# Kernel optimization log

Measured on AMD Instinct MI355X. Metric: run time of the kernel, lower is better.

## Reference

```python
import jax, jax.numpy as jnp
import numpy as np

B, N, D = 4, 1024, 1024      # batch, seq_len, query_dim
H, DH = 16, 64               # heads, dim_head; inner = H*DH = 1024
INNER = H * DH
SCALE = DH ** -0.5


def setup_inputs() -> dict:
    key = jax.random.key(0)
    ks = jax.random.split(key, 8)
    x = jax.random.normal(ks[0], (B, N, D), dtype=jnp.float32)
    rel_pos = jax.random.normal(ks[1], (B * H, N, N), dtype=jnp.float32)
    query_mask = jax.random.randint(ks[2], (B, N), 0, 2).astype(bool)
    context_mask = jax.random.randint(ks[3], (B, N), 0, 2).astype(bool)
    # Linear weights stored (in, out); to_q/to_kv have no bias, to_out has bias.
    Wq = jax.random.normal(ks[4], (D, INNER), dtype=jnp.float32) / np.sqrt(D)
    Wkv = jax.random.normal(ks[5], (D, 2 * INNER), dtype=jnp.float32) / np.sqrt(D)
    Wo = jax.random.normal(ks[6], (INNER, D), dtype=jnp.float32) / np.sqrt(INNER)
    bo = jax.random.normal(ks[7], (D,), dtype=jnp.float32) * 0.01
    return {"x": x, "rel_pos": rel_pos, "query_mask": query_mask,
            "context_mask": context_mask, "Wq": Wq, "Wkv": Wkv, "Wo": Wo, "bo": bo}


def reference(x, rel_pos, query_mask, context_mask, Wq, Wkv, Wo, bo):
    # Self-attention (context = x)
    q = x @ Wq                                 # [B, N, INNER]
    kv = x @ Wkv                               # [B, N, 2*INNER]
    k, v = jnp.split(kv, 2, axis=-1)
    # (b n (h d)) -> (b h n d)
    split_heads = lambda t: t.reshape(B, N, H, DH).transpose(0, 2, 1, 3)
    q, k, v = map(split_heads, (q, k, v))
    sim = jnp.einsum('bhid,bhjd->bhij', q, k) * SCALE
    sim = sim + rel_pos.reshape(B, H, N, N)
    neg = -jnp.finfo(sim.dtype).max
    # query_mask: (b i) -> mask rows; context_mask: (b j) -> mask cols
    sim = jnp.where(query_mask[:, None, :, None], sim, neg)
    sim = jnp.where(context_mask[:, None, None, :], sim, neg)
    attn = jax.nn.softmax(sim, axis=-1)
    out = jnp.einsum('bhij,bhjd->bhid', attn, v)    # [B, H, N, DH]
    out = out.transpose(0, 2, 1, 3).reshape(B, N, INNER)
    return out @ Wo + bo
```

## Files before the change

kernel.cpp:

```cpp
#include <hip/hip_runtime.h>


#define NEGMAX 3.402823466e+38f

typedef short short8 __attribute__((ext_vector_type(8)));
typedef float f32x4 __attribute__((ext_vector_type(4)));

__device__ __forceinline__ unsigned short f2bf(float f) {
  unsigned int u = __float_as_uint(f);
  u += 0x7FFFu + ((u >> 16) & 1u);
  return (unsigned short)(u >> 16);
}

__device__ __forceinline__ void stage16(const void* g, void* lds_base, int lane) {
#if __has_builtin(__builtin_amdgcn_global_load_lds)
  __builtin_amdgcn_global_load_lds(
      (const __attribute__((address_space(1))) unsigned int*)g,
      (__attribute__((address_space(3))) unsigned int*)lds_base, 16, 0, 0);
#else
  *(int4*)((char*)lds_base + lane * 16) = *(const int4*)g;
#endif
}

__global__ void cast_x_k(const float* __restrict__ x, unsigned short* __restrict__ xb) {
  int i = (blockIdx.x * 256 + threadIdx.x) * 4;
  float4 v = *(const float4*)(x + i);
  ushort4 o;
  o.x = f2bf(v.x); o.y = f2bf(v.y); o.z = f2bf(v.z); o.w = f2bf(v.w);
  *(ushort4*)(xb + i) = o;
}

__global__ __launch_bounds__(256) void tcast_k(const float* __restrict__ src, int ldsrc,
                                               unsigned short* __restrict__ dst) {
  __shared__ float T[64][65];
  const int n0 = blockIdx.x * 64, d0 = blockIdx.y * 64;
  const int tx = threadIdx.x & 63, ty = threadIdx.x >> 6;
#pragma unroll
  for (int k = 0; k < 16; ++k) {
    int dl = k * 4 + ty;
    T[dl][tx] = src[(size_t)(d0 + dl) * ldsrc + n0 + tx];
  }
  __syncthreads();
#pragma unroll
  for (int k = 0; k < 16; ++k) {
    int nl = k * 4 + ty;
    dst[(size_t)(n0 + nl) * 1024 + d0 + tx] = f2bf(T[tx][nl]);
  }
}

template <int MODE>
__global__ __launch_bounds__(256) void gemm_bt_k(
    const unsigned short* __restrict__ A, const unsigned short* __restrict__ Bt,
    unsigned short* __restrict__ qws, unsigned short* __restrict__ kws,
    unsigned short* __restrict__ vtws,
    const float* __restrict__ bias, float* __restrict__ Cout) {
  constexpr int K = 1024;
  constexpr int NKB = K / 32;
  __shared__ alignas(16) unsigned short As[128 * 32];
  __shared__ alignas(16) unsigned short Bs[128 * 32];
  const int tid = threadIdx.x;
  const int lane = tid & 63, w = tid >> 6;
  const int quad = lane >> 4, lanelo = lane & 15;
  const int tRow = blockIdx.y * 128, tCol = blockIdx.x * 128;
  const int wr = (w >> 1) * 64, wc = (w & 1) * 64;
  const char* AgB = (const char*)(A + (size_t)tRow * K);
  const char* BgB = (const char*)(Bt + (size_t)tCol * K);
  const int c0 = tid, c1 = tid + 256;
  const size_t a0off = (size_t)(c0 >> 2) * 2048 + (c0 & 3) * 16;
  const size_t a1off = (size_t)(c1 >> 2) * 2048 + (c1 & 3) * 16;
  char* ldsA0 = (char*)As + w * 1024;
  char* ldsA1 = (char*)As + 4096 + w * 1024;
  char* ldsB0 = (char*)Bs + w * 1024;
  char* ldsB1 = (char*)Bs + 4096 + w * 1024;

  f32x4 acc[4][4];
#pragma unroll
  for (int i = 0; i < 4; ++i)
#pragma unroll
    for (int j = 0; j < 4; ++j) acc[i][j] = (f32x4){0.f, 0.f, 0.f, 0.f};

  for (int kb = 0; kb < NKB; ++kb) {
    if (kb) __syncthreads();
    const size_t ko = (size_t)kb * 64;
    stage16(AgB + a0off + ko, ldsA0, lane);
    stage16(AgB + a1off + ko, ldsA1, lane);
    stage16(BgB + a0off + ko, ldsB0, lane);
    stage16(BgB + a1off + ko, ldsB1, lane);
    __syncthreads();

    short8 af[4], bf[4];
#pragma unroll
    for (int i = 0; i < 4; ++i)
      af[i] = *(const short8*)(As + (wr + i * 16 + lanelo) * 32 + quad * 8);
#pragma unroll
    for (int j = 0; j < 4; ++j)
      bf[j] = *(const short8*)(Bs + (wc + j * 16 + lanelo) * 32 + quad * 8);
#pragma unroll
    for (int i = 0; i < 4; ++i)
#pragma unroll
      for (int j = 0; j < 4; ++j)
        acc[i][j] = __builtin_amdgcn_mfma_f32_16x16x32_bf16(af[i], bf[j], acc[i][j], 0, 0, 0);
  }

  if (MODE == 0) {
#pragma unroll
    for (int i = 0; i < 4; ++i) {
      int row = tRow + wr + i * 16 + quad * 4;
      int b_ = row >> 10;
      int npos = row & 1023;
#pragma unroll
      for (int j = 0; j < 4; ++j) {
        int col = tCol + wc + j * 16 + lanelo;
        if (col < 2048) {
          unsigned short* dst = (col < 1024) ? qws : kws;
          int c = col & 1023;
          int hh = c >> 6, dh = c & 63;
          size_t base = ((size_t)(b_ * 16 + hh) * 1024 + npos) * 64 + dh;
#pragma unroll
          for (int r = 0; r < 4; ++r) dst[base + (size_t)r * 64] = f2bf(acc[i][j][r]);
        } else {
          int c = col - 2048;
          ushort4 pk;
          pk.x = f2bf(acc[i][j][0]);
          pk.y = f2bf(acc[i][j][1]);
          pk.z = f2bf(acc[i][j][2]);
          pk.w = f2bf(acc[i][j][3]);
          *(ushort4*)&vtws[((size_t)(b_ * 16 + (c >> 6)) * 64 + (c & 63)) * 1024 + npos] = pk;
        }
      }
    }
  } else {
#pragma unroll
    for (int i = 0; i < 4; ++i) {
      int row = tRow + wr + i * 16 + quad * 4;
#pragma unroll
      for (int j = 0; j < 4; ++j) {
        int col = tCol + wc + j * 16 + lanelo;
        float bv = bias[col];
#pragma unroll
        for (int r = 0; r < 4; ++r)
          Cout[(size_t)(row + r) * 1024 + col] = acc[i][j][r] + bv;
      }
    }
  }
}

__global__ __launch_bounds__(256) void attn_k(
    const unsigned short* __restrict__ q_ws, const unsigned short* __restrict__ k_ws,
    const unsigned short* __restrict__ vt_ws, const float* __restrict__ rel,
    const int* __restrict__ qmask, const int* __restrict__ cmask,
    unsigned short* __restrict__ aout) {
  constexpr float SCALE = 0.125f;
  __shared__ alignas(16) unsigned short Kl[64 * 72];
  __shared__ alignas(16) unsigned short Vl[64 * 72];
  __shared__ alignas(16) unsigned short Pl[4 * 16 * 72];
  __shared__ float cml[1024];

  const int tid = threadIdx.x;
  const int w = tid >> 6, lane = tid & 63;
  const int quad = lane >> 4, lanelo = lane & 15;
  const int bh = blockIdx.y, b_ = bh >> 4, h = bh & 15;
  const int qrow0 = blockIdx.x * 64 + w * 16;

  for (int i = tid; i < 1024; i += 256)
    cml[i] = (cmask[b_ * 1024 + i] != 0) ? 1.f : 0.f;

  const unsigned short* qg = q_ws + ((size_t)bh * 1024 + qrow0) * 64;
  short8 qf0 = *(const short8*)(qg + (size_t)lanelo * 64 + quad * 8);
  short8 qf1 = *(const short8*)(qg + (size_t)lanelo * 64 + 32 + quad * 8);

  float qmv[4];
#pragma unroll
  for (int r = 0; r < 4; ++r)
    qmv[r] = (qmask[b_ * 1024 + qrow0 + quad * 4 + r] != 0) ? 1.f : 0.f;

  f32x4 o[4];
#pragma unroll
  for (int g = 0; g < 4; ++g) o[g] = (f32x4){0.f, 0.f, 0.f, 0.f};
  float m_run[4], l_run[4];
#pragma unroll
  for (int r = 0; r < 4; ++r) { m_run[r] = -NEGMAX; l_run[r] = 0.f; }

  const char* kgB = (const char*)(k_ws + (size_t)bh * 65536);
  const char* vgB = (const char*)(vt_ws + (size_t)bh * 65536);
  const float* relg = rel + ((size_t)bh * 1024 + qrow0) * 1024;
  unsigned short* pw = Pl + w * 16 * 72;

  const int k0 = tid >> 3, ch0 = tid & 7;
  int4 kc0 = *(const int4*)(kgB + (size_t)k0 * 128 + ch0 * 16);
  int4 kc1 = *(const int4*)(kgB + (size_t)(k0 + 32) * 128 + ch0 * 16);
  int4 vc0 = *(const int4*)(vgB + (size_t)k0 * 2048 + ch0 * 16);
  int4 vc1 = *(const int4*)(vgB + (size_t)(k0 + 32) * 2048 + ch0 * 16);

  float rl[4][4];
#pragma unroll
  for (int r = 0; r < 4; ++r)
#pragma unroll
    for (int c = 0; c < 4; ++c)
      rl[r][c] = relg[(size_t)(quad * 4 + r) * 1024 + c * 16 + lanelo];

  for (int kb = 0; kb < 16; ++kb) {
    __syncthreads();
    *(int4*)((char*)Kl + k0 * 144 + ch0 * 16) = kc0;
    *(int4*)((char*)Kl + (k0 + 32) * 144 + ch0 * 16) = kc1;
    *(int4*)((char*)Vl + k0 * 144 + ch0 * 16) = vc0;
    *(int4*)((char*)Vl + (k0 + 32) * 144 + ch0 * 16) = vc1;
    __syncthreads();
    if (kb + 1 < 16) {
      const size_t kof = (size_t)(kb + 1) * 64;
      kc0 = *(const int4*)(kgB + (kof + k0) * 128 + ch0 * 16);
      kc1 = *(const int4*)(kgB + (kof + k0 + 32) * 128 + ch0 * 16);
      vc0 = *(const int4*)(vgB + (size_t)k0 * 2048 + kof * 2 + ch0 * 16);
      vc1 = *(const int4*)(vgB + (size_t)(k0 + 32) * 2048 + kof * 2 + ch0 * 16);
    }

    f32x4 s[4];
#pragma unroll
    for (int c = 0; c < 4; ++c) {
      s[c] = (f32x4){0.f, 0.f, 0.f, 0.f};
      short8 kfa = *(const short8*)((const char*)Kl + (c * 16 + lanelo) * 144 + quad * 16);
      s[c] = __builtin_amdgcn_mfma_f32_16x16x32_bf16(qf0, kfa, s[c], 0, 0, 0);
      short8 kfb = *(const short8*)((const char*)Kl + (c * 16 + lanelo) * 144 + 64 + quad * 16);
      s[c] = __builtin_amdgcn_mfma_f32_16x16x32_bf16(qf1, kfb, s[c], 0, 0, 0);
    }

    float rln[4][4];
    if (kb + 1 < 16) {
#pragma unroll
      for (int r = 0; r < 4; ++r)
#pragma unroll
        for (int c = 0; c < 4; ++c)
          rln[r][c] = relg[(size_t)(quad * 4 + r) * 1024 + (kb + 1) * 64 + c * 16 + lanelo];
    }

    float cm[4];
#pragma unroll
    for (int c = 0; c < 4; ++c) cm[c] = cml[kb * 64 + c * 16 + lanelo];

#pragma unroll
    for (int r = 0; r < 4; ++r) {
      const bool qok = qmv[r] != 0.f;
      float x[4], mloc = -NEGMAX;
#pragma unroll
      for (int c = 0; c < 4; ++c) {
        x[c] = (qok && cm[c] != 0.f) ? s[c][r] * SCALE + rl[r][c] : -NEGMAX;
        mloc = fmaxf(mloc, x[c]);
      }
      for (int off = 1; off < 16; off <<= 1) mloc = fmaxf(mloc, __shfl_xor(mloc, off));
      float mnew = fmaxf(m_run[r], mloc);
      float alpha = __expf(m_run[r] - mnew);
      m_run[r] = mnew;
      float ps = 0.f;
      unsigned short pb[4];
#pragma unroll
      for (int c = 0; c < 4; ++c) {
        float p = __expf(x[c] - mnew);
        ps += p;
        pb[c] = f2bf(p);
      }
      for (int off = 1; off < 16; off <<= 1) ps += __shfl_xor(ps, off);
      l_run[r] = l_run[r] * alpha + ps;
#pragma unroll
      for (int g = 0; g < 4; ++g) o[g][r] *= alpha;
#pragma unroll
      for (int c = 0; c < 4; ++c) pw[(quad * 4 + r) * 72 + c * 16 + lanelo] = pb[c];
    }

    if (kb + 1 < 16) {
#pragma unroll
      for (int r = 0; r < 4; ++r)
#pragma unroll
        for (int c = 0; c < 4; ++c) rl[r][c] = rln[r][c];
    }

#pragma unroll
    for (int c2 = 0; c2 < 2; ++c2) {
      short8 pa = *(const short8*)((const char*)pw + lanelo * 144 + c2 * 64 + quad * 16);
#pragma unroll
      for (int g = 0; g < 4; ++g) {
        short8 vb = *(const short8*)((const char*)Vl + (g * 16 + lanelo) * 144 + c2 * 64 + quad * 16);
        o[g] = __builtin_amdgcn_mfma_f32_16x16x32_bf16(pa, vb, o[g], 0, 0, 0);
      }
    }
  }

#pragma unroll
  for (int r = 0; r < 4; ++r) {
    float inv = 1.f / l_run[r];
    size_t row = (size_t)(b_ * 1024 + qrow0 + quad * 4 + r) * 1024;
#pragma unroll
    for (int g = 0; g < 4; ++g)
      aout[row + h * 64 + g * 16 + lanelo] = f2bf(o[g][r] * inv);
  }
}

extern "C" void kernel_launch(void* const* d_in, const int* in_sizes, int n_in,
                              void* d_out, int out_size, void* d_ws, size_t ws_size,
                              hipStream_t stream) {
  const float* x = (const float*)d_in[0];
  const float* rel = (const float*)d_in[1];
  const int* qmask = (const int*)d_in[2];
  const int* cmask = (const int*)d_in[3];
  const float* Wq = (const float*)d_in[4];
  const float* Wkv = (const float*)d_in[5];
  const float* Wo = (const float*)d_in[6];
  const float* bo = (const float*)d_in[7];
  float* out = (float*)d_out;

  char* ws = (char*)d_ws;
  const size_t MB = 1024 * 1024;
  unsigned short* w3t = (unsigned short*)(ws);
  unsigned short* wot = (unsigned short*)(ws + 6 * MB);
  unsigned short* xb  = (unsigned short*)(ws + 8 * MB);
  unsigned short* qws = (unsigned short*)(ws + 16 * MB);
  unsigned short* kws = (unsigned short*)(ws + 24 * MB);
  unsigned short* vtws = (unsigned short*)(ws + 32 * MB);
  unsigned short* aout = xb;

  cast_x_k<<<4096, 256, 0, stream>>>(x, xb);
  tcast_k<<<dim3(16, 16), 256, 0, stream>>>(Wq, 1024, w3t);
  tcast_k<<<dim3(32, 16), 256, 0, stream>>>(Wkv, 2048, w3t + (size_t)1024 * 1024);
  tcast_k<<<dim3(16, 16), 256, 0, stream>>>(Wo, 1024, wot);
  gemm_bt_k<0><<<dim3(24, 32), 256, 0, stream>>>(xb, w3t, qws, kws, vtws, nullptr, nullptr);
  attn_k<<<dim3(16, 64), 256, 0, stream>>>(qws, kws, vtws, rel, qmask, cmask, aout);
  gemm_bt_k<1><<<dim3(8, 32), 256, 0, stream>>>(aout, wot, nullptr, nullptr, nullptr, bo, out);
}
```

Before: 493.9 us.

## Use single-wave attention blocks loading K/V fragments directly from global memory

The attention kernel drops from four-wave blocks that cooperatively staged K and V tiles in LDS to single-wave blocks of 16 query rows. Each wave now reads its K and V MFMA fragments straight from global memory and also reads the context mask from global, which removes both __syncthreads per key block and the LDS staging. In exchange, K/V reuse across the four query waves that shared a tile is lost, so global/L2 traffic for K and V roughly quadruples. Nothing is prefetched a block ahead, so K/V load latency is exposed unless the higher block count hides it.

```diff
diff --git a/kernel.cpp b/kernel.cpp
--- a/kernel.cpp
+++ b/kernel.cpp
@@ -145,35 +145,33 @@
   }
 }
 
-__global__ __launch_bounds__(256) void attn_k(
+__global__ __launch_bounds__(64) void attn_k(
     const unsigned short* __restrict__ q_ws, const unsigned short* __restrict__ k_ws,
     const unsigned short* __restrict__ vt_ws, const float* __restrict__ rel,
     const int* __restrict__ qmask, const int* __restrict__ cmask,
     unsigned short* __restrict__ aout) {
   constexpr float SCALE = 0.125f;
-  __shared__ alignas(16) unsigned short Kl[64 * 72];
-  __shared__ alignas(16) unsigned short Vl[64 * 72];
-  __shared__ alignas(16) unsigned short Pl[4 * 16 * 72];
-  __shared__ float cml[1024];
-
-  const int tid = threadIdx.x;
-  const int w = tid >> 6, lane = tid & 63;
+  __shared__ alignas(16) unsigned short Pl[16 * 72];
+
+  const int lane = threadIdx.x;
   const int quad = lane >> 4, lanelo = lane & 15;
   const int bh = blockIdx.y, b_ = bh >> 4, h = bh & 15;
-  const int qrow0 = blockIdx.x * 64 + w * 16;
-
-  for (int i = tid; i < 1024; i += 256)
-    cml[i] = (cmask[b_ * 1024 + i] != 0) ? 1.f : 0.f;
+  const int qrow0 = blockIdx.x * 16;
 
   const unsigned short* qg = q_ws + ((size_t)bh * 1024 + qrow0) * 64;
-  short8 qf0 = *(const short8*)(qg + (size_t)lanelo * 64 + quad * 8);
-  short8 qf1 = *(const short8*)(qg + (size_t)lanelo * 64 + 32 + quad * 8);
+  short8 qf0 = *(const short8*)(qg + lanelo * 64 + quad * 8);
+  short8 qf1 = *(const short8*)(qg + lanelo * 64 + 32 + quad * 8);
 
   float qmv[4];
 #pragma unroll
   for (int r = 0; r < 4; ++r)
     qmv[r] = (qmask[b_ * 1024 + qrow0 + quad * 4 + r] != 0) ? 1.f : 0.f;
 
+  const unsigned short* kg = k_ws + (size_t)bh * 65536;
+  const unsigned short* vg = vt_ws + (size_t)bh * 65536;
+  const float* relg = rel + ((size_t)bh * 1024 + qrow0) * 1024;
+  const int* cmg = cmask + b_ * 1024;
+
   f32x4 o[4];
 #pragma unroll
   for (int g = 0; g < 4; ++g) o[g] = (f32x4){0.f, 0.f, 0.f, 0.f};
@@ -181,61 +179,50 @@
 #pragma unroll
   for (int r = 0; r < 4; ++r) { m_run[r] = -NEGMAX; l_run[r] = 0.f; }
 
-  const char* kgB = (const char*)(k_ws + (size_t)bh * 65536);
-  const char* vgB = (const char*)(vt_ws + (size_t)bh * 65536);
-  const float* relg = rel + ((size_t)bh * 1024 + qrow0) * 1024;
-  unsigned short* pw = Pl + w * 16 * 72;
-
-  const int k0 = tid >> 3, ch0 = tid & 7;
-  int4 kc0 = *(const int4*)(kgB + (size_t)k0 * 128 + ch0 * 16);
-  int4 kc1 = *(const int4*)(kgB + (size_t)(k0 + 32) * 128 + ch0 * 16);
-  int4 vc0 = *(const int4*)(vgB + (size_t)k0 * 2048 + ch0 * 16);
-  int4 vc1 = *(const int4*)(vgB + (size_t)(k0 + 32) * 2048 + ch0 * 16);
-
-  float rl[4][4];
+  float rl[4][4], cmv[4];
 #pragma unroll
   for (int r = 0; r < 4; ++r)
 #pragma unroll
     for (int c = 0; c < 4; ++c)
       rl[r][c] = relg[(size_t)(quad * 4 + r) * 1024 + c * 16 + lanelo];
+#pragma unroll
+  for (int c = 0; c < 4; ++c) cmv[c] = (cmg[c * 16 + lanelo] != 0) ? 1.f : 0.f;
 
   for (int kb = 0; kb < 16; ++kb) {
-    __syncthreads();
-    *(int4*)((char*)Kl + k0 * 144 + ch0 * 16) = kc0;
-    *(int4*)((char*)Kl + (k0 + 32) * 144 + ch0 * 16) = kc1;
-    *(int4*)((char*)Vl + k0 * 144 + ch0 * 16) = vc0;
-    *(int4*)((char*)Vl + (k0 + 32) * 144 + ch0 * 16) = vc1;
-    __syncthreads();
-    if (kb + 1 < 16) {
-      const size_t kof = (size_t)(kb + 1) * 64;
-      kc0 = *(const int4*)(kgB + (kof + k0) * 128 + ch0 * 16);
-      kc1 = *(const int4*)(kgB + (kof + k0 + 32) * 128 + ch0 * 16);
-      vc0 = *(const int4*)(vgB + (size_t)k0 * 2048 + kof * 2 + ch0 * 16);
-      vc1 = *(const int4*)(vgB + (size_t)(k0 + 32) * 2048 + kof * 2 + ch0 * 16);
-    }
+    const int ko = kb * 64;
+
+    short8 kf0[4], kf1[4];
+#pragma unroll
+    for (int c = 0; c < 4; ++c) {
+      const unsigned short* kr = kg + (size_t)(ko + c * 16 + lanelo) * 64 + quad * 8;
+      kf0[c] = *(const short8*)(kr);
+      kf1[c] = *(const short8*)(kr + 32);
+    }
+    short8 vf[4][2];
+#pragma unroll
+    for (int g = 0; g < 4; ++g)
+#pragma unroll
+      for (int c2 = 0; c2 < 2; ++c2)
+        vf[g][c2] = *(const short8*)(vg + (size_t)(g * 16 + lanelo) * 1024 + ko + c2 * 32 + quad * 8);
 
     f32x4 s[4];
 #pragma unroll
     for (int c = 0; c < 4; ++c) {
       s[c] = (f32x4){0.f, 0.f, 0.f, 0.f};
-      short8 kfa = *(const short8*)((const char*)Kl + (c * 16 + lanelo) * 144 + quad * 16);
-      s[c] = __builtin_amdgcn_mfma_f32_16x16x32_bf16(qf0, kfa, s[c], 0, 0, 0);
-      short8 kfb = *(const short8*)((const char*)Kl + (c * 16 + lanelo) * 144 + 64 + quad * 16);
-      s[c] = __builtin_amdgcn_mfma_f32_16x16x32_bf16(qf1, kfb, s[c], 0, 0, 0);
-    }
-
-    float rln[4][4];
+      s[c] = __builtin_amdgcn_mfma_f32_16x16x32_bf16(qf0, kf0[c], s[c], 0, 0, 0);
+      s[c] = __builtin_amdgcn_mfma_f32_16x16x32_bf16(qf1, kf1[c], s[c], 0, 0, 0);
+    }
+
+    float rn[4][4], cn[4];
     if (kb + 1 < 16) {
 #pragma unroll
       for (int r = 0; r < 4; ++r)
 #pragma unroll
         for (int c = 0; c < 4; ++c)
-          rln[r][c] = relg[(size_t)(quad * 4 + r) * 1024 + (kb + 1) * 64 + c * 16 + lanelo];
-    }
-
-    float cm[4];
-#pragma unroll
-    for (int c = 0; c < 4; ++c) cm[c] = cml[kb * 64 + c * 16 + lanelo];
+          rn[r][c] = relg[(size_t)(quad * 4 + r) * 1024 + ko + 64 + c * 16 + lanelo];
+#pragma unroll
+      for (int c = 0; c < 4; ++c) cn[c] = (cmg[ko + 64 + c * 16 + lanelo] != 0) ? 1.f : 0.f;
+    }
 
 #pragma unroll
     for (int r = 0; r < 4; ++r) {
@@ -243,7 +230,7 @@
       float x[4], mloc = -NEGMAX;
 #pragma unroll
       for (int c = 0; c < 4; ++c) {
-        x[c] = (qok && cm[c] != 0.f) ? s[c][r] * SCALE + rl[r][c] : -NEGMAX;
+        x[c] = (qok && cmv[c] != 0.f) ? s[c][r] * SCALE + rl[r][c] : -NEGMAX;
         mloc = fmaxf(mloc, x[c]);
       }
       for (int off = 1; off < 16; off <<= 1) mloc = fmaxf(mloc, __shfl_xor(mloc, off));
@@ -263,24 +250,24 @@
 #pragma unroll
       for (int g = 0; g < 4; ++g) o[g][r] *= alpha;
 #pragma unroll
-      for (int c = 0; c < 4; ++c) pw[(quad * 4 + r) * 72 + c * 16 + lanelo] = pb[c];
+      for (int c = 0; c < 4; ++c) Pl[(quad * 4 + r) * 72 + c * 16 + lanelo] = pb[c];
     }
 
     if (kb + 1 < 16) {
 #pragma unroll
       for (int r = 0; r < 4; ++r)
 #pragma unroll
-        for (int c = 0; c < 4; ++c) rl[r][c] = rln[r][c];
+        for (int c = 0; c < 4; ++c) rl[r][c] = rn[r][c];
+#pragma unroll
+      for (int c = 0; c < 4; ++c) cmv[c] = cn[c];
     }
 
 #pragma unroll
     for (int c2 = 0; c2 < 2; ++c2) {
-      short8 pa = *(const short8*)((const char*)pw + lanelo * 144 + c2 * 64 + quad * 16);
-#pragma unroll
-      for (int g = 0; g < 4; ++g) {
-        short8 vb = *(const short8*)((const char*)Vl + (g * 16 + lanelo) * 144 + c2 * 64 + quad * 16);
-        o[g] = __builtin_amdgcn_mfma_f32_16x16x32_bf16(pa, vb, o[g], 0, 0, 0);
-      }
+      short8 pa = *(const short8*)((const char*)Pl + lanelo * 144 + c2 * 64 + quad * 16);
+#pragma unroll
+      for (int g = 0; g < 4; ++g)
+        o[g] = __builtin_amdgcn_mfma_f32_16x16x32_bf16(pa, vf[g][c2], o[g], 0, 0, 0);
     }
   }
 
@@ -322,6 +309,6 @@
   tcast_k<<<dim3(32, 16), 256, 0, stream>>>(Wkv, 2048, w3t + (size_t)1024 * 1024);
   tcast_k<<<dim3(16, 16), 256, 0, stream>>>(Wo, 1024, wot);
   gemm_bt_k<0><<<dim3(24, 32), 256, 0, stream>>>(xb, w3t, qws, kws, vtws, nullptr, nullptr);
-  attn_k<<<dim3(16, 64), 256, 0, stream>>>(qws, kws, vtws, rel, qmask, cmask, aout);
+  attn_k<<<dim3(64, 64), 64, 0, stream>>>(qws, kws, vtws, rel, qmask, cmask, aout);
   gemm_bt_k<1><<<dim3(8, 32), 256, 0, stream>>>(aout, wot, nullptr, nullptr, nullptr, bo, out);
 }
```

New measurement: 526.6 us. 6.6% more time.
